# Kernel optimization log

Hardware: AMD Instinct MI355X
Metric: run time of the kernel (lower is better)

## Reference

```python
import jax, jax.numpy as jnp
import numpy as np

B, C, N, H = 16, 256, 2048, 128


def setup_inputs() -> dict:
    key = jax.random.key(0)
    ks = jax.random.split(key, 9)
    s_in = 1.0 / np.sqrt(C)
    s_h = 1.0 / np.sqrt(H)
    return {
        "x": jax.random.normal(ks[0], (B, C, N), dtype=jnp.float32),
        "Wq": jax.random.uniform(ks[1], (H, C), jnp.float32, -s_in, s_in),
        "bq": jax.random.uniform(ks[2], (H,), jnp.float32, -s_in, s_in),
        "Wk": jax.random.uniform(ks[3], (H, C), jnp.float32, -s_in, s_in),
        "bk": jax.random.uniform(ks[4], (H,), jnp.float32, -s_in, s_in),
        "Wv": jax.random.uniform(ks[5], (H, C), jnp.float32, -s_in, s_in),
        "bv": jax.random.uniform(ks[6], (H,), jnp.float32, -s_in, s_in),
        "Wf": jax.random.uniform(ks[7], (C, H), jnp.float32, -s_h, s_h),
        "bf": jax.random.uniform(ks[8], (C,), jnp.float32, -s_h, s_h),
    }


def reference(x, Wq, bq, Wk, bk, Wv, bv, Wf, bf):
    # 1x1 conv == channel-wise linear: [B,C,N] -> [B,H,N]
    Q = jnp.einsum("bcn,hc->bhn", x, Wq) + bq[:, None]
    K = jnp.einsum("bcn,hc->bhn", x, Wk) + bk[:, None]
    V = jnp.einsum("bcn,hc->bhn", x, Wv) + bv[:, None]
    # attn[b, i, j] = softmax_j( Q[b,:,i] . K[b,:,j] )   (no sqrt(d) scaling, as in source)
    scores = jnp.einsum("bhi,bhj->bij", Q, K)          # [B, N, N]
    attn = jax.nn.softmax(scores, axis=-1)
    # out[b, h, i] = sum_j V[b,h,j] * attn[b,i,j]
    out = jnp.einsum("bhj,bij->bhi", V, attn)           # [B, H, N]
    out = jnp.einsum("bhn,ch->bcn", out, Wf) + bf[:, None]
    return out + x
```

## Files before the change

### kernel.cpp

```cpp
#include <hip/hip_runtime.h>
#include <hip/hip_bf16.h>

#define BATCH 16
#define CDIM 256
#define NDIM 2048
#define HDIM 128
#define KVB 64
#define NT (NDIM / KVB)

typedef __bf16 bf16;
typedef float f32x4 __attribute__((ext_vector_type(4)));
typedef float f32x16 __attribute__((ext_vector_type(16)));
typedef bf16 bf16x8 __attribute__((ext_vector_type(8)));
typedef unsigned int u32x4 __attribute__((ext_vector_type(4)));

#define LOG2E 1.4426950408889634f

__device__ __forceinline__ int swz512(int row, int colbyte) {
  return row * 512 + (colbyte ^ ((row & 15) << 4));
}
__device__ __forceinline__ int swz256(int row, int colbyte) {
  return row * 256 + (colbyte ^ ((row & 7) << 4));
}

__device__ __forceinline__ f32x4 mfma16(bf16x8 a, bf16x8 b, f32x4 c) {
  return __builtin_amdgcn_mfma_f32_16x16x32_bf16(a, b, c, 0, 0, 0);
}
__device__ __forceinline__ f32x16 mfma32(bf16x8 a, bf16x8 b, f32x16 c) {
  return __builtin_amdgcn_mfma_f32_32x32x16_bf16(a, b, c, 0, 0, 0);
}

__device__ __forceinline__ unsigned cvtpk(float lo, float hi) {
  unsigned r;
  asm("v_cvt_pk_bf16_f32 %0, %1, %2" : "=v"(r) : "v"(lo), "v"(hi));
  return r;
}
__device__ __forceinline__ void pswap(unsigned &a, unsigned &b) {
  asm volatile("v_permlane32_swap_b32 %0, %1" : "+v"(a), "+v"(b));
}

__device__ __forceinline__ void gload16(const bf16* g, char* l) {
  __builtin_amdgcn_global_load_lds(
      (const __attribute__((address_space(1))) void*)g,
      (__attribute__((address_space(3))) void*)l, 16, 0, 0);
}

__device__ __forceinline__ bf16x8 cvt8(float4 a, float4 b) {
  bf16x8 o;
  o[0] = (bf16)a.x; o[1] = (bf16)a.y; o[2] = (bf16)a.z; o[3] = (bf16)a.w;
  o[4] = (bf16)b.x; o[5] = (bf16)b.y; o[6] = (bf16)b.z; o[7] = (bf16)b.w;
  return o;
}

__global__ __launch_bounds__(256) void k1_qkv(
    const float* __restrict__ x,
    const float* __restrict__ Wq, const float* __restrict__ bq,
    const float* __restrict__ Wk, const float* __restrict__ bk,
    const float* __restrict__ Wv, const float* __restrict__ bv,
    bf16* __restrict__ Qo, bf16* __restrict__ Ko, bf16* __restrict__ Vo) {
  __shared__ char lds[65536];
  char* xT = lds;
  char* Wt = lds + 32768;

  const int t = threadIdx.x;
  const int l = t & 63;
  const int w = t >> 6;
  const int b = blockIdx.x >> 5;
  const int n0 = (blockIdx.x & 31) * 64;

#pragma unroll
  for (int pass = 0; pass < 16; ++pass) {
    int c = pass * 16 + (t >> 4);
    int nq = t & 15;
    const float4 v = *reinterpret_cast<const float4*>(
        x + (size_t)(b * CDIM + c) * NDIM + n0 + nq * 4);
    float fv[4] = {v.x, v.y, v.z, v.w};
#pragma unroll
    for (int i = 0; i < 4; ++i) {
      int row = nq * 4 + i;
      *reinterpret_cast<bf16*>(xT + swz512(row, c * 2)) = (bf16)fv[i];
    }
  }

  const float* Wp[3] = {Wq, Wk, Wv};
  const float* bp[3] = {bq, bk, bv};

#pragma unroll 1
  for (int p = 0; p < 3; ++p) {
    f32x4 acc[8];
#pragma unroll
    for (int i = 0; i < 8; ++i) acc[i] = f32x4{0.f, 0.f, 0.f, 0.f};

#pragma unroll 1
    for (int kh = 0; kh < 2; ++kh) {
      __syncthreads();
#pragma unroll
      for (int pass = 0; pass < 8; ++pass) {
        int h = pass * 16 + (t >> 4);
        int cq = t & 15;
        const float* src = Wp[p] + (size_t)h * CDIM + kh * 128 + cq * 8;
        float4 v0 = *reinterpret_cast<const float4*>(src);
        float4 v1 = *reinterpret_cast<const float4*>(src + 4);
        *reinterpret_cast<bf16x8*>(Wt + swz256(h, cq * 16)) = cvt8(v0, v1);
      }
      __syncthreads();

      if (p < 2) {
#pragma unroll
        for (int ks = 0; ks < 4; ++ks) {
          int cb2 = ks * 64 + (l >> 4) * 16;
          bf16x8 a = *reinterpret_cast<const bf16x8*>(
              xT + swz512(w * 16 + (l & 15), kh * 256 + cb2));
#pragma unroll
          for (int nf = 0; nf < 8; ++nf) {
            bf16x8 bb = *reinterpret_cast<const bf16x8*>(
                Wt + swz256(nf * 16 + (l & 15), cb2));
            acc[nf] = mfma16(a, bb, acc[nf]);
          }
        }
      } else {
#pragma unroll
        for (int ks = 0; ks < 4; ++ks) {
          int cb2 = ks * 64 + (l >> 4) * 16;
          bf16x8 a0 = *reinterpret_cast<const bf16x8*>(
              Wt + swz256(w * 32 + (l & 15), cb2));
          bf16x8 a1 = *reinterpret_cast<const bf16x8*>(
              Wt + swz256(w * 32 + 16 + (l & 15), cb2));
#pragma unroll
          for (int nf = 0; nf < 4; ++nf) {
            bf16x8 bb = *reinterpret_cast<const bf16x8*>(
                xT + swz512(nf * 16 + (l & 15), kh * 256 + cb2));
            acc[nf] = mfma16(a0, bb, acc[nf]);
            acc[4 + nf] = mfma16(a1, bb, acc[4 + nf]);
          }
        }
      }
    }

    if (p < 2) {
      bf16* dst = (p == 0) ? Qo : Ko;
#pragma unroll
      for (int nf = 0; nf < 8; ++nf) {
        float bias = bp[p][nf * 16 + (l & 15)];
#pragma unroll
        for (int r = 0; r < 4; ++r) {
          int n = n0 + w * 16 + (l >> 4) * 4 + r;
          int h = nf * 16 + (l & 15);
          dst[(size_t)(b * NDIM + n) * HDIM + h] = (bf16)(acc[nf][r] + bias);
        }
      }
    } else {
#pragma unroll
      for (int mf = 0; mf < 2; ++mf)
#pragma unroll
        for (int nf = 0; nf < 4; ++nf)
#pragma unroll
          for (int r = 0; r < 4; ++r) {
            int h = w * 32 + mf * 16 + (l >> 4) * 4 + r;
            int n = n0 + nf * 16 + (l & 15);
            Vo[(size_t)(b * HDIM + h) * NDIM + n] =
                (bf16)(acc[mf * 4 + nf][r] + bp[2][h]);
          }
    }
  }
}

__global__ __launch_bounds__(256, 2) void k2_attn(
    const bf16* __restrict__ Q, const bf16* __restrict__ K,
    const bf16* __restrict__ V, bf16* __restrict__ O) {
  extern __shared__ char lds[];

  const int t = threadIdx.x;
  const int l = t & 63;
  const int w = t >> 6;
  const int wm = w & 1;
  const int wk = w >> 1;
  const int hi = l >> 5;
  const int c31 = l & 31;

  const int pid = blockIdx.x;
  const int b = (pid & 7) * 2 + ((pid >> 3) >> 5);
  const int q0 = ((pid >> 3) & 31) * 64;

  bf16x8 qf[8];
  {
    const bf16* qb = Q + ((size_t)b * NDIM + q0 + wm * 32 + c31) * HDIM + hi * 8;
#pragma unroll
    for (int cs = 0; cs < 8; ++cs)
      qf[cs] = *reinterpret_cast<const bf16x8*>(qb + cs * 16);
  }

  unsigned offK[4], offV[4];
  {
    const int krow = w * 16 + (l >> 4);
    const int kslot = l & 15;
#pragma unroll
    for (int i = 0; i < 4; ++i) {
      int r = krow + i * 4;
      offK[i] = (unsigned)((b * NDIM + r) * HDIM + (kslot ^ (r & 15)) * 8);
    }
    const int vrow = w * 32 + (l >> 3);
    const int vslot = l & 7;
#pragma unroll
    for (int i = 0; i < 4; ++i) {
      int r = vrow + i * 8;
      offV[i] = (unsigned)((b * HDIM + r) * NDIM + (vslot ^ (r & 7)) * 8);
    }
  }
  const int kbase = w * 4096;
  const int vbase = 16384 + w * 4096;

  f32x16 oacc[4];
#pragma unroll
  for (int dg = 0; dg < 4; ++dg)
#pragma unroll
    for (int r = 0; r < 16; ++r) oacc[dg][r] = 0.f;
  float l_run = 0.f;

#pragma unroll
  for (int i = 0; i < 4; ++i) gload16(K + offK[i], lds + kbase + i * 1024);
#pragma unroll
  for (int i = 0; i < 4; ++i) gload16(V + offV[i], lds + vbase + i * 1024);

  const int krow = wk * 32 + c31;
  const int rxk = krow & 15;
  const int rxv = c31 & 7;

#pragma unroll 1
  for (int kt = 0; kt < NT; ++kt) {
    char* buf = lds + (kt & 1) * 32768;
    if (kt + 1 < NT) {
      char* nbuf = lds + ((kt + 1) & 1) * 32768;
#pragma unroll
      for (int i = 0; i < 4; ++i) {
        offK[i] += (unsigned)(KVB * HDIM);
        gload16(K + offK[i], nbuf + kbase + i * 1024);
      }
#pragma unroll
      for (int i = 0; i < 4; ++i) {
        offV[i] += (unsigned)KVB;
        gload16(V + offV[i], nbuf + vbase + i * 1024);
      }
      asm volatile("s_waitcnt vmcnt(8)" ::: "memory");
    } else {
      asm volatile("s_waitcnt vmcnt(0)" ::: "memory");
    }
    __builtin_amdgcn_s_barrier();

    const char* Kt = buf;
    const char* Vt = buf + 16384;

    f32x16 s;
#pragma unroll
    for (int r = 0; r < 16; ++r) s[r] = 0.f;
    __builtin_amdgcn_s_setprio(1);
    {
      const char* kr = Kt + krow * 256;
#pragma unroll
      for (int cs = 0; cs < 8; ++cs) {
        bf16x8 kf = *reinterpret_cast<const bf16x8*>(
            kr + (((cs * 2 + hi) ^ rxk) * 16));
        s = mfma32(kf, qf[cs], s);
      }
    }
    __builtin_amdgcn_s_setprio(0);

    float sum = 0.f;
#pragma unroll
    for (int r = 0; r < 16; ++r) {
      float p = __builtin_amdgcn_exp2f(s[r] * LOG2E);
      s[r] = p;
      sum += p;
    }
    l_run += sum;

    unsigned w0 = cvtpk(s[0], s[1]);
    unsigned w1 = cvtpk(s[2], s[3]);
    unsigned w2 = cvtpk(s[4], s[5]);
    unsigned w3 = cvtpk(s[6], s[7]);
    unsigned w4 = cvtpk(s[8], s[9]);
    unsigned w5 = cvtpk(s[10], s[11]);
    unsigned w6 = cvtpk(s[12], s[13]);
    unsigned w7 = cvtpk(s[14], s[15]);
    pswap(w0, w2); pswap(w1, w3); pswap(w4, w6); pswap(w5, w7);
    u32x4 pw0 = {w0, w1, w2, w3};
    u32x4 pw1 = {w4, w5, w6, w7};
    bf16x8 pa0 = __builtin_bit_cast(bf16x8, pw0);
    bf16x8 pa1 = __builtin_bit_cast(bf16x8, pw1);

    __builtin_amdgcn_s_setprio(1);
#pragma unroll
    for (int dg = 0; dg < 4; ++dg) {
      const char* vr = Vt + (dg * 32 + c31) * 128;
      bf16x8 vf0 = *reinterpret_cast<const bf16x8*>(
          vr + (((wk * 4 + 0 + hi) ^ rxv) * 16));
      oacc[dg] = mfma32(pa0, vf0, oacc[dg]);
      bf16x8 vf1 = *reinterpret_cast<const bf16x8*>(
          vr + (((wk * 4 + 2 + hi) ^ rxv) * 16));
      oacc[dg] = mfma32(pa1, vf1, oacc[dg]);
    }
    __builtin_amdgcn_s_setprio(0);
    __builtin_amdgcn_s_barrier();
  }

  l_run += __shfl_xor(l_run, 32);
  float* O1 = (float*)lds;
  float* L1 = (float*)(lds + 32768);
  if (wk == 1) {
#pragma unroll
    for (int dg = 0; dg < 4; ++dg)
#pragma unroll
      for (int r = 0; r < 16; ++r)
        O1[wm * 4096 + (dg * 16 + r) * 64 + l] = oacc[dg][r];
    if (l < 32) L1[wm * 32 + c31] = l_run;
  }
  __syncthreads();
  if (wk == 0) {
    float linv = 1.0f / (l_run + L1[wm * 32 + c31]);
    int ibits = __builtin_bit_cast(int, linv);
#pragma unroll
    for (int dg = 0; dg < 4; ++dg) {
      int h = dg * 32 + c31;
#pragma unroll
      for (int r = 0; r < 16; ++r) {
        int crow = (r & 3) + 8 * (r >> 2) + 4 * hi;
        float fr = __builtin_bit_cast(
            float, __builtin_amdgcn_ds_bpermute(crow * 4, ibits));
        float val = (oacc[dg][r] + O1[wm * 4096 + (dg * 16 + r) * 64 + l]) * fr;
        int n = q0 + wm * 32 + crow;
        O[((size_t)b * NDIM + n) * HDIM + h] = (bf16)val;
      }
    }
  }
}

__global__ __launch_bounds__(256) void k3_proj(
    const bf16* __restrict__ O, const float* __restrict__ Wf,
    const float* __restrict__ bfv, const float* __restrict__ x,
    float* __restrict__ out) {
  __shared__ char lds[49152];
  char* Wt = lds;
  char* Ot = lds + 32768;

  const int t = threadIdx.x;
  const int l = t & 63;
  const int w = t >> 6;
  const int b = blockIdx.x >> 5;
  const int n0 = (blockIdx.x & 31) * 64;

#pragma unroll
  for (int pass = 0; pass < 4; ++pass) {
    int n = pass * 16 + (t >> 4);
    int hq = t & 15;
    uint4 d = *reinterpret_cast<const uint4*>(
        O + (size_t)(b * NDIM + n0 + n) * HDIM + hq * 8);
    *reinterpret_cast<uint4*>(Ot + swz256(n, hq * 16)) = d;
  }

#pragma unroll 1
  for (int ch = 0; ch < 2; ++ch) {
    __syncthreads();
#pragma unroll
    for (int pass = 0; pass < 8; ++pass) {
      int cl = pass * 16 + (t >> 4);
      int hq = t & 15;
      const float* src = Wf + (size_t)(ch * 128 + cl) * HDIM + hq * 8;
      float4 v0 = *reinterpret_cast<const float4*>(src);
      float4 v1 = *reinterpret_cast<const float4*>(src + 4);
      *reinterpret_cast<bf16x8*>(Wt + swz256(cl, hq * 16)) = cvt8(v0, v1);
    }
    __syncthreads();

    f32x4 acc[2][4];
#pragma unroll
    for (int i = 0; i < 2; ++i)
#pragma unroll
      for (int j = 0; j < 4; ++j) acc[i][j] = f32x4{0.f, 0.f, 0.f, 0.f};

#pragma unroll
    for (int ks = 0; ks < 4; ++ks) {
      int cb = ks * 64 + (l >> 4) * 16;
      bf16x8 a0 = *reinterpret_cast<const bf16x8*>(
          Wt + swz256(w * 32 + (l & 15), cb));
      bf16x8 a1 = *reinterpret_cast<const bf16x8*>(
          Wt + swz256(w * 32 + 16 + (l & 15), cb));
#pragma unroll
      for (int nf = 0; nf < 4; ++nf) {
        bf16x8 bb = *reinterpret_cast<const bf16x8*>(
            Ot + swz256(nf * 16 + (l & 15), cb));
        acc[0][nf] = mfma16(a0, bb, acc[0][nf]);
        acc[1][nf] = mfma16(a1, bb, acc[1][nf]);
      }
    }

#pragma unroll
    for (int mf = 0; mf < 2; ++mf)
#pragma unroll
      for (int nf = 0; nf < 4; ++nf)
#pragma unroll
        for (int r = 0; r < 4; ++r) {
          int c = ch * 128 + w * 32 + mf * 16 + (l >> 4) * 4 + r;
          int n = n0 + nf * 16 + (l & 15);
          size_t idx = (size_t)(b * CDIM + c) * NDIM + n;
          out[idx] = acc[mf][nf][r] + bfv[c] + x[idx];
        }
  }
}

extern "C" void kernel_launch(void* const* d_in, const int* in_sizes, int n_in,
                              void* d_out, int out_size, void* d_ws,
                              size_t ws_size, hipStream_t stream) {
  (void)in_sizes; (void)n_in; (void)out_size;
  const float* x = (const float*)d_in[0];
  const float* Wq = (const float*)d_in[1];
  const float* bq = (const float*)d_in[2];
  const float* Wk = (const float*)d_in[3];
  const float* bk = (const float*)d_in[4];
  const float* Wv = (const float*)d_in[5];
  const float* bv = (const float*)d_in[6];
  const float* Wf = (const float*)d_in[7];
  const float* bfv = (const float*)d_in[8];
  float* out = (float*)d_out;

  if (ws_size < (24u << 20)) return;
  char* ws = (char*)d_ws;
  bf16* Qb = (bf16*)(ws);
  bf16* Kb = (bf16*)(ws + (8u << 20));
  bf16* Vb = (bf16*)(ws + (16u << 20));

  const unsigned k2_lds = 65536;
  hipFuncSetAttribute(reinterpret_cast<const void*>(k2_attn),
                      hipFuncAttributeMaxDynamicSharedMemorySize, (int)k2_lds);

  k1_qkv<<<512, 256, 0, stream>>>(x, Wq, bq, Wk, bk, Wv, bv, Qb, Kb, Vb);
  k2_attn<<<512, 256, k2_lds, stream>>>(Qb, Kb, Vb, Qb);
  k3_proj<<<512, 256, 0, stream>>>(Qb, Wf, bfv, x, out);
}
```

Measured before the change: 95.46 us.

## Pre-pack QKV weights, fuse QKV projection, and enlarge attention tiles to 512 threads

A new prep kernel converts Wq/Wk/Wv to bf16 in MFMA fragment order and stores them in the tail of the output buffer, which k3 later overwrites. The QKV kernel then computes all three projections in a single pass with no per-pass weight staging in LDS. It also transposes x through lane shuffles and declares an occupancy hint of 3. The attention kernel moves to 512-thread blocks, each handling 128 queries with KV tiles of 128, so every K/V tile is reused across twice as many queries. This costs a larger LDS footprint (about 130KB) and a longer four-way cross-warp reduction at the end.

```diff
diff --git a/kernel.cpp b/kernel.cpp
--- a/kernel.cpp
+++ b/kernel.cpp
@@ -5,7 +5,7 @@
 #define CDIM 256
 #define NDIM 2048
 #define HDIM 128
-#define KVB 64
+#define KVB 128
 #define NT (NDIM / KVB)
 
 typedef __bf16 bf16;
@@ -13,6 +13,7 @@
 typedef float f32x16 __attribute__((ext_vector_type(16)));
 typedef bf16 bf16x8 __attribute__((ext_vector_type(8)));
 typedef unsigned int u32x4 __attribute__((ext_vector_type(4)));
+typedef unsigned int u32x2 __attribute__((ext_vector_type(2)));
 
 #define LOG2E 1.4426950408889634f
 
@@ -52,120 +53,114 @@
   return o;
 }
 
-__global__ __launch_bounds__(256) void k1_qkv(
-    const float* __restrict__ x,
-    const float* __restrict__ Wq, const float* __restrict__ bq,
-    const float* __restrict__ Wk, const float* __restrict__ bk,
-    const float* __restrict__ Wv, const float* __restrict__ bv,
+__global__ __launch_bounds__(256) void k0_prep(
+    const float* __restrict__ Wq, const float* __restrict__ Wk,
+    const float* __restrict__ Wv, bf16* __restrict__ blk) {
+  int tg = blockIdx.x * 256 + threadIdx.x;
+  int f = tg >> 6, l = tg & 63;
+  const float* W = (f < 64) ? Wq : (f < 128 ? Wk : Wv);
+  int ks = (f >> 3) & 7, hb = f & 7;
+  const float* src = W + (size_t)(hb * 16 + (l & 15)) * CDIM + ks * 32 + (l >> 4) * 8;
+  float4 v0 = *reinterpret_cast<const float4*>(src);
+  float4 v1 = *reinterpret_cast<const float4*>(src + 4);
+  *reinterpret_cast<bf16x8*>(blk + f * 512 + l * 8) = cvt8(v0, v1);
+}
+
+__global__ __launch_bounds__(256, 3) void k1_qkv(
+    const float* __restrict__ x, const bf16* __restrict__ blk,
+    const float* __restrict__ bq, const float* __restrict__ bk,
+    const float* __restrict__ bv,
     bf16* __restrict__ Qo, bf16* __restrict__ Ko, bf16* __restrict__ Vo) {
-  __shared__ char lds[65536];
-  char* xT = lds;
-  char* Wt = lds + 32768;
+  __shared__ char xT[32768];
 
   const int t = threadIdx.x;
   const int l = t & 63;
   const int w = t >> 6;
+  const int q = (l >> 4) & 3;
   const int b = blockIdx.x >> 5;
   const int n0 = (blockIdx.x & 31) * 64;
 
 #pragma unroll
-  for (int pass = 0; pass < 16; ++pass) {
-    int c = pass * 16 + (t >> 4);
-    int nq = t & 15;
-    const float4 v = *reinterpret_cast<const float4*>(
-        x + (size_t)(b * CDIM + c) * NDIM + n0 + nq * 4);
-    float fv[4] = {v.x, v.y, v.z, v.w};
-#pragma unroll
-    for (int i = 0; i < 4; ++i) {
-      int row = nq * 4 + i;
-      *reinterpret_cast<bf16*>(xT + swz512(row, c * 2)) = (bf16)fv[i];
-    }
-  }
-
-  const float* Wp[3] = {Wq, Wk, Wv};
-  const float* bp[3] = {bq, bk, bv};
-
-#pragma unroll 1
-  for (int p = 0; p < 3; ++p) {
-    f32x4 acc[8];
-#pragma unroll
-    for (int i = 0; i < 8; ++i) acc[i] = f32x4{0.f, 0.f, 0.f, 0.f};
-
-#pragma unroll 1
-    for (int kh = 0; kh < 2; ++kh) {
-      __syncthreads();
-#pragma unroll
-      for (int pass = 0; pass < 8; ++pass) {
-        int h = pass * 16 + (t >> 4);
-        int cq = t & 15;
-        const float* src = Wp[p] + (size_t)h * CDIM + kh * 128 + cq * 8;
-        float4 v0 = *reinterpret_cast<const float4*>(src);
-        float4 v1 = *reinterpret_cast<const float4*>(src + 4);
-        *reinterpret_cast<bf16x8*>(Wt + swz256(h, cq * 16)) = cvt8(v0, v1);
-      }
-      __syncthreads();
-
-      if (p < 2) {
-#pragma unroll
-        for (int ks = 0; ks < 4; ++ks) {
-          int cb2 = ks * 64 + (l >> 4) * 16;
-          bf16x8 a = *reinterpret_cast<const bf16x8*>(
-              xT + swz512(w * 16 + (l & 15), kh * 256 + cb2));
-#pragma unroll
-          for (int nf = 0; nf < 8; ++nf) {
-            bf16x8 bb = *reinterpret_cast<const bf16x8*>(
-                Wt + swz256(nf * 16 + (l & 15), cb2));
-            acc[nf] = mfma16(a, bb, acc[nf]);
-          }
-        }
-      } else {
-#pragma unroll
-        for (int ks = 0; ks < 4; ++ks) {
-          int cb2 = ks * 64 + (l >> 4) * 16;
-          bf16x8 a0 = *reinterpret_cast<const bf16x8*>(
-              Wt + swz256(w * 32 + (l & 15), cb2));
-          bf16x8 a1 = *reinterpret_cast<const bf16x8*>(
-              Wt + swz256(w * 32 + 16 + (l & 15), cb2));
-#pragma unroll
-          for (int nf = 0; nf < 4; ++nf) {
-            bf16x8 bb = *reinterpret_cast<const bf16x8*>(
-                xT + swz512(nf * 16 + (l & 15), kh * 256 + cb2));
-            acc[nf] = mfma16(a0, bb, acc[nf]);
-            acc[4 + nf] = mfma16(a1, bb, acc[4 + nf]);
-          }
-        }
-      }
-    }
-
-    if (p < 2) {
-      bf16* dst = (p == 0) ? Qo : Ko;
-#pragma unroll
-      for (int nf = 0; nf < 8; ++nf) {
-        float bias = bp[p][nf * 16 + (l & 15)];
-#pragma unroll
-        for (int r = 0; r < 4; ++r) {
-          int n = n0 + w * 16 + (l >> 4) * 4 + r;
-          int h = nf * 16 + (l & 15);
-          dst[(size_t)(b * NDIM + n) * HDIM + h] = (bf16)(acc[nf][r] + bias);
-        }
-      }
-    } else {
-#pragma unroll
-      for (int mf = 0; mf < 2; ++mf)
-#pragma unroll
-        for (int nf = 0; nf < 4; ++nf)
-#pragma unroll
-          for (int r = 0; r < 4; ++r) {
-            int h = w * 32 + mf * 16 + (l >> 4) * 4 + r;
-            int n = n0 + nf * 16 + (l & 15);
-            Vo[(size_t)(b * HDIM + h) * NDIM + n] =
-                (bf16)(acc[mf * 4 + nf][r] + bp[2][h]);
-          }
-    }
-  }
-}
-
-__global__ __launch_bounds__(256, 2) void k2_attn(
+  for (int p = 0; p < 16; ++p) {
+    int c = w * 64 + p * 4 + q;
+    float4 v = *reinterpret_cast<const float4*>(
+        x + (size_t)(b * CDIM + c) * NDIM + n0 + (l & 15) * 4);
+    float t0 = __shfl_xor(v.x, 16), t1 = __shfl_xor(v.y, 16);
+    float t2 = __shfl_xor(v.z, 16), t3 = __shfl_xor(v.w, 16);
+    float4 wv;
+    if ((q & 1) == 0) wv = make_float4(v.x, t0, v.z, t2);
+    else              wv = make_float4(t1, v.y, t3, v.w);
+    float s0 = __shfl_xor(wv.x, 32), s1 = __shfl_xor(wv.y, 32);
+    float s2 = __shfl_xor(wv.z, 32), s3 = __shfl_xor(wv.w, 32);
+    float4 z;
+    if ((q & 2) == 0) z = make_float4(wv.x, wv.y, s0, s1);
+    else              z = make_float4(s2, s3, wv.z, wv.w);
+    u32x2 pk = {cvtpk(z.x, z.y), cvtpk(z.z, z.w)};
+    int n = (l & 15) * 4 + q;
+    int slot = w * 8 + (p >> 1);
+    *reinterpret_cast<u32x2*>(
+        xT + n * 512 + ((slot ^ (n & 15)) * 16 + (p & 1) * 8)) = pk;
+  }
+  __syncthreads();
+
+  const bf16* bq_ = blk;
+  const bf16* bk_ = blk + 64 * 512;
+  const bf16* bv_ = blk + 128 * 512;
+
+  f32x4 aq[8], ak[8], av[8];
+#pragma unroll
+  for (int i = 0; i < 8; ++i) {
+    aq[i] = f32x4{0.f, 0.f, 0.f, 0.f};
+    ak[i] = f32x4{0.f, 0.f, 0.f, 0.f};
+    av[i] = f32x4{0.f, 0.f, 0.f, 0.f};
+  }
+
+#pragma unroll
+  for (int ks = 0; ks < 8; ++ks) {
+    bf16x8 a = *reinterpret_cast<const bf16x8*>(
+        xT + swz512(w * 16 + (l & 15), ks * 64 + (l >> 4) * 16));
+#pragma unroll
+    for (int nf = 0; nf < 8; ++nf) {
+      bf16x8 wq = *reinterpret_cast<const bf16x8*>(bq_ + (ks * 8 + nf) * 512 + l * 8);
+      aq[nf] = mfma16(a, wq, aq[nf]);
+      bf16x8 wk = *reinterpret_cast<const bf16x8*>(bk_ + (ks * 8 + nf) * 512 + l * 8);
+      ak[nf] = mfma16(a, wk, ak[nf]);
+    }
+    bf16x8 wv0 = *reinterpret_cast<const bf16x8*>(bv_ + (ks * 8 + w * 2 + 0) * 512 + l * 8);
+    bf16x8 wv1 = *reinterpret_cast<const bf16x8*>(bv_ + (ks * 8 + w * 2 + 1) * 512 + l * 8);
+#pragma unroll
+    for (int nf4 = 0; nf4 < 4; ++nf4) {
+      bf16x8 bx = *reinterpret_cast<const bf16x8*>(
+          xT + swz512(nf4 * 16 + (l & 15), ks * 64 + (l >> 4) * 16));
+      av[nf4] = mfma16(wv0, bx, av[nf4]);
+      av[4 + nf4] = mfma16(wv1, bx, av[4 + nf4]);
+    }
+  }
+
+#pragma unroll
+  for (int nf = 0; nf < 8; ++nf) {
+    int h = nf * 16 + (l & 15);
+    float biasq = bq[h], biask = bk[h];
+#pragma unroll
+    for (int r = 0; r < 4; ++r) {
+      int n = n0 + w * 16 + (l >> 4) * 4 + r;
+      Qo[(size_t)(b * NDIM + n) * HDIM + h] = (bf16)(aq[nf][r] + biasq);
+      Ko[(size_t)(b * NDIM + n) * HDIM + h] = (bf16)(ak[nf][r] + biask);
+    }
+  }
+#pragma unroll
+  for (int mf = 0; mf < 2; ++mf)
+#pragma unroll
+    for (int nf4 = 0; nf4 < 4; ++nf4)
+#pragma unroll
+      for (int r = 0; r < 4; ++r) {
+        int h = w * 32 + mf * 16 + (l >> 4) * 4 + r;
+        int n = n0 + nf4 * 16 + (l & 15);
+        Vo[(size_t)(b * HDIM + h) * NDIM + n] = (bf16)(av[mf * 4 + nf4][r] + bv[h]);
+      }
+}
+
+__global__ __launch_bounds__(512, 1) void k2_attn(
     const bf16* __restrict__ Q, const bf16* __restrict__ K,
     const bf16* __restrict__ V, bf16* __restrict__ O) {
   extern __shared__ char lds[];
@@ -179,67 +174,59 @@
   const int c31 = l & 31;
 
   const int pid = blockIdx.x;
-  const int b = (pid & 7) * 2 + ((pid >> 3) >> 5);
-  const int q0 = ((pid >> 3) & 31) * 64;
-
-  bf16x8 qf[8];
+  const int b = (pid & 7) * 2 + ((pid >> 3) >> 4);
+  const int q0 = ((pid >> 3) & 15) * 128;
+
+  bf16x8 qf0[8], qf1[8];
   {
-    const bf16* qb = Q + ((size_t)b * NDIM + q0 + wm * 32 + c31) * HDIM + hi * 8;
-#pragma unroll
-    for (int cs = 0; cs < 8; ++cs)
-      qf[cs] = *reinterpret_cast<const bf16x8*>(qb + cs * 16);
-  }
-
+    const bf16* qb = Q + ((size_t)b * NDIM + q0 + wm * 64 + c31) * HDIM + hi * 8;
+#pragma unroll
+    for (int cs = 0; cs < 8; ++cs) {
+      qf0[cs] = *reinterpret_cast<const bf16x8*>(qb + cs * 16);
+      qf1[cs] = *reinterpret_cast<const bf16x8*>(qb + 32 * HDIM + cs * 16);
+    }
+  }
+
+  const int srow = w * 4 + (l >> 4);
+  const int slot = l & 15;
   unsigned offK[4], offV[4];
-  {
-    const int krow = w * 16 + (l >> 4);
-    const int kslot = l & 15;
-#pragma unroll
-    for (int i = 0; i < 4; ++i) {
-      int r = krow + i * 4;
-      offK[i] = (unsigned)((b * NDIM + r) * HDIM + (kslot ^ (r & 15)) * 8);
-    }
-    const int vrow = w * 32 + (l >> 3);
-    const int vslot = l & 7;
-#pragma unroll
-    for (int i = 0; i < 4; ++i) {
-      int r = vrow + i * 8;
-      offV[i] = (unsigned)((b * HDIM + r) * NDIM + (vslot ^ (r & 7)) * 8);
-    }
-  }
-  const int kbase = w * 4096;
-  const int vbase = 16384 + w * 4096;
-
-  f32x16 oacc[4];
+#pragma unroll
+  for (int i = 0; i < 4; ++i) {
+    int r = srow + i * 32;
+    offK[i] = (unsigned)((b * NDIM + r) * HDIM + (slot ^ (r & 15)) * 8);
+    offV[i] = (unsigned)((b * HDIM + r) * NDIM + (slot ^ (r & 15)) * 8);
+  }
+  const int kdst = w * 1024;
+  const int vdst = 32768 + w * 1024;
+
+  f32x16 oacc0[4], oacc1[4];
 #pragma unroll
   for (int dg = 0; dg < 4; ++dg)
 #pragma unroll
-    for (int r = 0; r < 16; ++r) oacc[dg][r] = 0.f;
-  float l_run = 0.f;
-
-#pragma unroll
-  for (int i = 0; i < 4; ++i) gload16(K + offK[i], lds + kbase + i * 1024);
-#pragma unroll
-  for (int i = 0; i < 4; ++i) gload16(V + offV[i], lds + vbase + i * 1024);
-
-  const int krow = wk * 32 + c31;
-  const int rxk = krow & 15;
-  const int rxv = c31 & 7;
+    for (int r = 0; r < 16; ++r) { oacc0[dg][r] = 0.f; oacc1[dg][r] = 0.f; }
+  float l0 = 0.f, l1 = 0.f;
+
+#pragma unroll
+  for (int i = 0; i < 4; ++i) gload16(K + offK[i], lds + kdst + i * 8192);
+#pragma unroll
+  for (int i = 0; i < 4; ++i) gload16(V + offV[i], lds + vdst + i * 8192);
+
+  const int rx = c31 & 15;
 
 #pragma unroll 1
   for (int kt = 0; kt < NT; ++kt) {
-    char* buf = lds + (kt & 1) * 32768;
+    char* buf = lds + (kt & 1) * 65536;
     if (kt + 1 < NT) {
-      char* nbuf = lds + ((kt + 1) & 1) * 32768;
+      char* nbuf = lds + ((kt + 1) & 1) * 65536;
 #pragma unroll
       for (int i = 0; i < 4; ++i) {
         offK[i] += (unsigned)(KVB * HDIM);
-        gload16(K + offK[i], nbuf + kbase + i * 1024);
+        gload16(K + offK[i], nbuf + kdst + i * 8192);
       }
 #pragma unroll
       for (int i = 0; i < 4; ++i) {
         offV[i] += (unsigned)KVB;
-        gload16(V + offV[i], nbuf + vbase + i * 1024);
+        gload16(V + offV[i], nbuf + vdst + i * 8192);
       }
       asm volatile("s_waitcnt vmcnt(8)" ::: "memory");
     } else {
@@ -248,87 +235,134 @@
     __builtin_amdgcn_s_barrier();
 
     const char* Kt = buf;
-    const char* Vt = buf + 16384;
-
-    f32x16 s;
-#pragma unroll
-    for (int r = 0; r < 16; ++r) s[r] = 0.f;
+    const char* Vt = buf + 32768;
+
+    f32x16 s0, s1;
+#pragma unroll
+    for (int r = 0; r < 16; ++r) { s0[r] = 0.f; s1[r] = 0.f; }
     __builtin_amdgcn_s_setprio(1);
     {
-      const char* kr = Kt + krow * 256;
+      const char* kr = Kt + (wk * 32 + c31) * 256;
 #pragma unroll
       for (int cs = 0; cs < 8; ++cs) {
         bf16x8 kf = *reinterpret_cast<const bf16x8*>(
-            kr + (((cs * 2 + hi) ^ rxk) * 16));
-        s = mfma32(kf, qf[cs], s);
+            kr + (((cs * 2 + hi) ^ rx) * 16));
+        s0 = mfma32(kf, qf0[cs], s0);
+        s1 = mfma32(kf, qf1[cs], s1);
       }
     }
     __builtin_amdgcn_s_setprio(0);
 
-    float sum = 0.f;
-#pragma unroll
-    for (int r = 0; r < 16; ++r) {
-      float p = __builtin_amdgcn_exp2f(s[r] * LOG2E);
-      s[r] = p;
-      sum += p;
-    }
-    l_run += sum;
-
-    unsigned w0 = cvtpk(s[0], s[1]);
-    unsigned w1 = cvtpk(s[2], s[3]);
-    unsigned w2 = cvtpk(s[4], s[5]);
-    unsigned w3 = cvtpk(s[6], s[7]);
-    unsigned w4 = cvtpk(s[8], s[9]);
-    unsigned w5 = cvtpk(s[10], s[11]);
-    unsigned w6 = cvtpk(s[12], s[13]);
-    unsigned w7 = cvtpk(s[14], s[15]);
-    pswap(w0, w2); pswap(w1, w3); pswap(w4, w6); pswap(w5, w7);
-    u32x4 pw0 = {w0, w1, w2, w3};
-    u32x4 pw1 = {w4, w5, w6, w7};
-    bf16x8 pa0 = __builtin_bit_cast(bf16x8, pw0);
-    bf16x8 pa1 = __builtin_bit_cast(bf16x8, pw1);
+    bf16x8 pa0[2], pa1[2];
+#pragma unroll
+    for (int qs = 0; qs < 2; ++qs) {
+      f32x16& s = qs ? s1 : s0;
+      float sum = 0.f;
+#pragma unroll
+      for (int r = 0; r < 16; ++r) {
+        float p = __builtin_amdgcn_exp2f(s[r] * LOG2E);
+        s[r] = p;
+        sum += p;
+      }
+      if (qs) l1 += sum; else l0 += sum;
+      unsigned w0 = cvtpk(s[0], s[1]);
+      unsigned w1 = cvtpk(s[2], s[3]);
+      unsigned w2 = cvtpk(s[4], s[5]);
+      unsigned w3 = cvtpk(s[6], s[7]);
+      unsigned w4 = cvtpk(s[8], s[9]);
+      unsigned w5 = cvtpk(s[10], s[11]);
+      unsigned w6 = cvtpk(s[12], s[13]);
+      unsigned w7 = cvtpk(s[14], s[15]);
+      pswap(w0, w2); pswap(w1, w3); pswap(w4, w6); pswap(w5, w7);
+      u32x4 pw0 = {w0, w1, w2, w3};
+      u32x4 pw1 = {w4, w5, w6, w7};
+      (qs ? pa1 : pa0)[0] = __builtin_bit_cast(bf16x8, pw0);
+      (qs ? pa1 : pa0)[1] = __builtin_bit_cast(bf16x8, pw1);
+    }
 
     __builtin_amdgcn_s_setprio(1);
 #pragma unroll
-    for (int dg = 0; dg < 4; ++dg) {
-      const char* vr = Vt + (dg * 32 + c31) * 128;
-      bf16x8 vf0 = *reinterpret_cast<const bf16x8*>(
-          vr + (((wk * 4 + 0 + hi) ^ rxv) * 16));
-      oacc[dg] = mfma32(pa0, vf0, oacc[dg]);
-      bf16x8 vf1 = *reinterpret_cast<const bf16x8*>(
-          vr + (((wk * 4 + 2 + hi) ^ rxv) * 16));
-      oacc[dg] = mfma32(pa1, vf1, oacc[dg]);
+    for (int ks = 0; ks < 2; ++ks) {
+#pragma unroll
+      for (int dg = 0; dg < 4; ++dg) {
+        const char* vr = Vt + (dg * 32 + c31) * 256;
+        bf16x8 vf = *reinterpret_cast<const bf16x8*>(
+            vr + (((wk * 4 + ks * 2 + hi) ^ rx) * 16));
+        oacc0[dg] = mfma32(pa0[ks], vf, oacc0[dg]);
+        oacc1[dg] = mfma32(pa1[ks], vf, oacc1[dg]);
+      }
     }
     __builtin_amdgcn_s_setprio(0);
     __builtin_amdgcn_s_barrier();
   }
 
-  l_run += __shfl_xor(l_run, 32);
-  float* O1 = (float*)lds;
-  float* L1 = (float*)(lds + 32768);
-  if (wk == 1) {
+  l0 += __shfl_xor(l0, 32);
+  l1 += __shfl_xor(l1, 32);
+  float* Ls = (float*)(lds + 131072);
+  if (l < 32) {
+    Ls[((wm * 2 + 0) * 4 + wk) * 32 + c31] = l0;
+    Ls[((wm * 2 + 1) * 4 + wk) * 32 + c31] = l1;
+  }
+  auto region = [&](int idx) { return (float*)(lds + idx * 32768); };
+  if (wk & 1) {
+    float* R = region(wm * 2 + (wk >> 1));
 #pragma unroll
     for (int dg = 0; dg < 4; ++dg)
 #pragma unroll
-      for (int r = 0; r < 16; ++r)
-        O1[wm * 4096 + (dg * 16 + r) * 64 + l] = oacc[dg][r];
-    if (l < 32) L1[wm * 32 + c31] = l_run;
+      for (int r = 0; r < 16; ++r) {
+        R[((0 * 4 + dg) * 16 + r) * 64 + l] = oacc0[dg][r];
+        R[((1 * 4 + dg) * 16 + r) * 64 + l] = oacc1[dg][r];
+      }
+  }
+  __syncthreads();
+  if (!(wk & 1)) {
+    float* R = region(wm * 2 + (wk >> 1));
+#pragma unroll
+    for (int dg = 0; dg < 4; ++dg)
+#pragma unroll
+      for (int r = 0; r < 16; ++r) {
+        oacc0[dg][r] += R[((0 * 4 + dg) * 16 + r) * 64 + l];
+        oacc1[dg][r] += R[((1 * 4 + dg) * 16 + r) * 64 + l];
+      }
+  }
+  __syncthreads();
+  if (wk == 2) {
+    float* R = region(wm);
+#pragma unroll
+    for (int dg = 0; dg < 4; ++dg)
+#pragma unroll
+      for (int r = 0; r < 16; ++r) {
+        R[((0 * 4 + dg) * 16 + r) * 64 + l] = oacc0[dg][r];
+        R[((1 * 4 + dg) * 16 + r) * 64 + l] = oacc1[dg][r];
+      }
   }
   __syncthreads();
   if (wk == 0) {
-    float linv = 1.0f / (l_run + L1[wm * 32 + c31]);
-    int ibits = __builtin_bit_cast(int, linv);
+    float* R = region(wm);
+    float linv0, linv1;
+    {
+      int base0 = (wm * 2 + 0) * 4 * 32 + c31;
+      int base1 = (wm * 2 + 1) * 4 * 32 + c31;
+      linv0 = 1.0f / (Ls[base0] + Ls[base0 + 32] + Ls[base0 + 64] + Ls[base0 + 96]);
+      linv1 = 1.0f / (Ls[base1] + Ls[base1 + 32] + Ls[base1 + 64] + Ls[base1 + 96]);
+    }
+    int ib0 = __builtin_bit_cast(int, linv0);
+    int ib1 = __builtin_bit_cast(int, linv1);
 #pragma unroll
     for (int dg = 0; dg < 4; ++dg) {
       int h = dg * 32 + c31;
 #pragma unroll
       for (int r = 0; r < 16; ++r) {
         int crow = (r & 3) + 8 * (r >> 2) + 4 * hi;
-        float fr = __builtin_bit_cast(
-            float, __builtin_amdgcn_ds_bpermute(crow * 4, ibits));
-        float val = (oacc[dg][r] + O1[wm * 4096 + (dg * 16 + r) * 64 + l]) * fr;
-        int n = q0 + wm * 32 + crow;
-        O[((size_t)b * NDIM + n) * HDIM + h] = (bf16)val;
+        float f0 = __builtin_bit_cast(
+            float, __builtin_amdgcn_ds_bpermute(crow * 4, ib0));
+        float f1 = __builtin_bit_cast(
+            float, __builtin_amdgcn_ds_bpermute(crow * 4, ib1));
+        float v0 = (oacc0[dg][r] + R[((0 * 4 + dg) * 16 + r) * 64 + l]) * f0;
+        float v1 = (oacc1[dg][r] + R[((1 * 4 + dg) * 16 + r) * 64 + l]) * f1;
+        int n_0 = q0 + wm * 64 + crow;
+        O[((size_t)b * NDIM + n_0) * HDIM + h] = (bf16)v0;
+        O[((size_t)b * NDIM + n_0 + 32) * HDIM + h] = (bf16)v1;
       }
     }
   }
@@ -410,7 +444,7 @@
 extern "C" void kernel_launch(void* const* d_in, const int* in_sizes, int n_in,
                               void* d_out, int out_size, void* d_ws,
                               size_t ws_size, hipStream_t stream) {
-  (void)in_sizes; (void)n_in; (void)out_size;
+  (void)in_sizes; (void)n_in;
   const float* x = (const float*)d_in[0];
   const float* Wq = (const float*)d_in[1];
   const float* bq = (const float*)d_in[2];
@@ -428,11 +462,15 @@
   bf16* Kb = (bf16*)(ws + (8u << 20));
   bf16* Vb = (bf16*)(ws + (16u << 20));
 
-  const unsigned k2_lds = 65536;
+  const size_t out_bytes = (size_t)out_size * 4;
+  bf16* Wblk = (bf16*)((char*)d_out + out_bytes - 196608);
+
+  const unsigned k2_lds = 133120;
   hipFuncSetAttribute(reinterpret_cast<const void*>(k2_attn),
                       hipFuncAttributeMaxDynamicSharedMemorySize, (int)k2_lds);
 
-  k1_qkv<<<512, 256, 0, stream>>>(x, Wq, bq, Wk, bk, Wv, bv, Qb, Kb, Vb);
-  k2_attn<<<512, 256, k2_lds, stream>>>(Qb, Kb, Vb, Qb);
+  k0_prep<<<48, 256, 0, stream>>>(Wq, Wk, Wv, Wblk);
+  k1_qkv<<<512, 256, 0, stream>>>(x, Wblk, bq, bk, bv, Qb, Kb, Vb);
+  k2_attn<<<256, 512, k2_lds, stream>>>(Qb, Kb, Vb, Qb);
   k3_proj<<<512, 256, 0, stream>>>(Qb, Wf, bfv, x, out);
 }
```

Result: slower. 125.7 us (+31.7%).
